# Performance work log

Measured on AMD Instinct MI355X. Metric: run time of the kernel, lower is better.

The kernel has to match this reference:

```python
import jax, jax.numpy as jnp
import numpy as np
import math

IN_CH = 256
OUT_CH = 256
N_JOINTS = 25
BATCH = 16384


def setup_inputs() -> dict:
    key = jax.random.key(0)
    kx, kw = jax.random.split(key)
    x = jax.random.normal(kx, (N_JOINTS, BATCH, IN_CH), dtype=jnp.float32)
    stdv = 1.0 / math.sqrt(OUT_CH)
    weight = jax.random.uniform(kw, (IN_CH, OUT_CH), dtype=jnp.float32,
                                minval=-stdv, maxval=stdv)
    return {"x": x, "weight": weight}


def reference(x, weight):
    # x: (N, B, D) -> attention over joints N per batch element
    xb = jnp.transpose(x, (1, 0, 2))            # (B, N, D)
    s3 = jnp.einsum('bnd,bmd->bnm', xb, xb)     # (B, N, N) self-similarity
    s = jax.nn.softmax(s3, axis=-1)
    out = jnp.einsum('bnm,bmd->bnd', s, xb)     # (B, N, D)
    out = out @ weight                           # (B, N, out_channels)
    return out
```

## Files before the change

### kernel.cpp

```cpp
#include <hip/hip_runtime.h>

#define GRID   512
#define BLOCK  512
#define BATCH  16384
#define NJ     25
#define DEPTH  256
#define ITERS  (BATCH / GRID)

typedef short s16x8 __attribute__((ext_vector_type(8)));
typedef short s16x4 __attribute__((ext_vector_type(4)));
typedef float f32x4 __attribute__((ext_vector_type(4)));

__device__ __forceinline__ short f2bf(float f) {
  union { float f; unsigned u; } c; c.f = f;
  unsigned r = (c.u + 0x7FFFu + ((c.u >> 16) & 1u)) >> 16;
  return (short)r;
}

#define MFMA(a, b, c) __builtin_amdgcn_mfma_f32_16x16x32_bf16((a), (b), (c), 0, 0, 0)

__global__ __launch_bounds__(BLOCK, 4)
void geo_gcn_fused(const float* __restrict__ x,
                   const float* __restrict__ w,
                   float* __restrict__ out)
{
  __shared__ short As[2][32][264];
  __shared__ short Ps[32][40];
  __shared__ float S3[32][33];
  __shared__ short Yt[8][32][40];

  const int tid  = threadIdx.x;
  const int wv   = tid >> 6;
  const int lane = tid & 63;
  const int quad = lane >> 4;
  const int l16  = lane & 15;

  s16x8 wf[8][2];
  {
    const int ncol = wv * 32 + l16;
#pragma unroll
    for (int ks = 0; ks < 8; ++ks)
#pragma unroll
      for (int td = 0; td < 2; ++td) {
        const float* wp = w + (size_t)(ks * 32 + quad * 8) * DEPTH + ncol + td * 16;
#pragma unroll
        for (int j = 0; j < 8; ++j)
          wf[ks][td][j] = f2bf(wp[(size_t)j * DEPTH]);
      }
  }

  const int srow = tid >> 4;
  const int sc   = tid & 15;
  const int tm_s = (wv >> 1) & 1;
  const int tn_s = wv & 1;

  const float* xrow = x + (size_t)srow * BATCH * DEPTH + sc * 16;

  {
    float4 c0 = make_float4(0.f, 0.f, 0.f, 0.f), c1 = c0, c2 = c0, c3 = c0;
    if (srow < NJ) {
      const float* xp = xrow + (size_t)blockIdx.x * DEPTH;
      c0 = *(const float4*)(xp + 0);  c1 = *(const float4*)(xp + 4);
      c2 = *(const float4*)(xp + 8);  c3 = *(const float4*)(xp + 12);
    }
    s16x8 h0, h1;
    h0[0]=f2bf(c0.x); h0[1]=f2bf(c0.y); h0[2]=f2bf(c0.z); h0[3]=f2bf(c0.w);
    h0[4]=f2bf(c1.x); h0[5]=f2bf(c1.y); h0[6]=f2bf(c1.z); h0[7]=f2bf(c1.w);
    h1[0]=f2bf(c2.x); h1[1]=f2bf(c2.y); h1[2]=f2bf(c2.z); h1[3]=f2bf(c2.w);
    h1[4]=f2bf(c3.x); h1[5]=f2bf(c3.y); h1[6]=f2bf(c3.z); h1[7]=f2bf(c3.w);
    *(s16x8*)&As[0][srow][sc * 16]     = h0;
    *(s16x8*)&As[0][srow][sc * 16 + 8] = h1;
  }
  __syncthreads();

  for (int ib = 0; ib < ITERS; ++ib) {
    const int b   = blockIdx.x + GRID * ib;
    const int buf = ib & 1;

    float4 n0 = make_float4(0.f, 0.f, 0.f, 0.f), n1 = n0, n2 = n0, n3 = n0;
    if ((ib + 1 < ITERS) && (srow < NJ)) {
      const float* xp = xrow + (size_t)(b + GRID) * DEPTH;
      n0 = *(const float4*)(xp + 0);  n1 = *(const float4*)(xp + 4);
      n2 = *(const float4*)(xp + 8);  n3 = *(const float4*)(xp + 12);
    }

    f32x4 sacc = (f32x4){0.f, 0.f, 0.f, 0.f};
    f32x4 yacc[2][2];
#pragma unroll
    for (int i = 0; i < 2; ++i)
#pragma unroll
      for (int j = 0; j < 2; ++j) yacc[i][j] = (f32x4){0.f, 0.f, 0.f, 0.f};

#pragma unroll
    for (int ks = 0; ks < 8; ++ks) {
      s16x8 a0 = *(const s16x8*)&As[buf][l16][ks * 32 + quad * 8];
      s16x8 a1 = *(const s16x8*)&As[buf][16 + l16][ks * 32 + quad * 8];
      if (wv < 4) sacc = MFMA(tm_s ? a1 : a0, tn_s ? a1 : a0, sacc);
      yacc[0][0] = MFMA(a0, wf[ks][0], yacc[0][0]);
      yacc[0][1] = MFMA(a0, wf[ks][1], yacc[0][1]);
      yacc[1][0] = MFMA(a1, wf[ks][0], yacc[1][0]);
      yacc[1][1] = MFMA(a1, wf[ks][1], yacc[1][1]);
    }

    if (wv < 4) {
#pragma unroll
      for (int r = 0; r < 4; ++r)
        S3[tm_s * 16 + quad * 4 + r][tn_s * 16 + l16] = sacc[r];
    }
    __syncthreads();

    if (tid < 256) {
      const int row = tid >> 3, c8 = tid & 7;
      float v[4]; float mx = -3.0e38f;
#pragma unroll
      for (int i = 0; i < 4; ++i) {
        const int j = c8 + 8 * i;
        v[i] = (j < NJ) ? S3[row][j] : -3.0e38f;
        mx = fmaxf(mx, v[i]);
      }
      mx = fmaxf(mx, __shfl_xor(mx, 1));
      mx = fmaxf(mx, __shfl_xor(mx, 2));
      mx = fmaxf(mx, __shfl_xor(mx, 4));
      float e[4]; float sum = 0.f;
#pragma unroll
      for (int i = 0; i < 4; ++i) {
        const int j = c8 + 8 * i;
        e[i] = (j < NJ) ? __expf(v[i] - mx) : 0.f;
        sum += e[i];
      }
      sum += __shfl_xor(sum, 1);
      sum += __shfl_xor(sum, 2);
      sum += __shfl_xor(sum, 4);
      const float rinv = 1.0f / sum;
#pragma unroll
      for (int i = 0; i < 4; ++i)
        Ps[row][c8 + 8 * i] = f2bf(e[i] * rinv);
    }
    __syncthreads();

#pragma unroll
    for (int tm = 0; tm < 2; ++tm)
#pragma unroll
      for (int td = 0; td < 2; ++td) {
        s16x4 hy;
#pragma unroll
        for (int r = 0; r < 4; ++r) hy[r] = f2bf(yacc[tm][td][r]);
        *(s16x4*)&Yt[wv][td * 16 + l16][tm * 16 + quad * 4] = hy;
      }

    s16x8 pf0 = *(const s16x8*)&Ps[l16][quad * 8];
    s16x8 pf1 = *(const s16x8*)&Ps[16 + l16][quad * 8];
    const f32x4 z4 = (f32x4){0.f, 0.f, 0.f, 0.f};
    float* ob = out + (size_t)b * NJ * DEPTH + wv * 32 + l16;
#pragma unroll
    for (int td = 0; td < 2; ++td) {
      s16x8 yb = *(const s16x8*)&Yt[wv][td * 16 + l16][quad * 8];
      f32x4 o0 = MFMA(pf0, yb, z4);
      f32x4 o1 = MFMA(pf1, yb, z4);
#pragma unroll
      for (int r = 0; r < 4; ++r) {
        ob[(size_t)(quad * 4 + r) * DEPTH + td * 16] = o0[r];
        const int nr = 16 + quad * 4 + r;
        if (nr < NJ) ob[(size_t)nr * DEPTH + td * 16] = o1[r];
      }
    }

    if (ib + 1 < ITERS) {
      s16x8 h0, h1;
      h0[0]=f2bf(n0.x); h0[1]=f2bf(n0.y); h0[2]=f2bf(n0.z); h0[3]=f2bf(n0.w);
      h0[4]=f2bf(n1.x); h0[5]=f2bf(n1.y); h0[6]=f2bf(n1.z); h0[7]=f2bf(n1.w);
      h1[0]=f2bf(n2.x); h1[1]=f2bf(n2.y); h1[2]=f2bf(n2.z); h1[3]=f2bf(n2.w);
      h1[4]=f2bf(n3.x); h1[5]=f2bf(n3.y); h1[6]=f2bf(n3.z); h1[7]=f2bf(n3.w);
      *(s16x8*)&As[1 - buf][srow][sc * 16]     = h0;
      *(s16x8*)&As[1 - buf][srow][sc * 16 + 8] = h1;
    }
    __syncthreads();
  }
}

extern "C" void kernel_launch(void* const* d_in, const int* in_sizes, int n_in,
                              void* d_out, int out_size, void* d_ws, size_t ws_size,
                              hipStream_t stream) {
  (void)in_sizes; (void)n_in; (void)out_size; (void)d_ws; (void)ws_size;
  const float* x = (const float*)d_in[0];
  const float* w = (const float*)d_in[1];
  float* out = (float*)d_out;
  geo_gcn_fused<<<dim3(GRID), dim3(BLOCK), 0, stream>>>(x, w, out);
}
```

Measured before the change: 793.5 us.

## Single-buffer swizzled LDS tiles and drop the end-of-iteration barrier

```diff
diff --git a/kernel.cpp b/kernel.cpp
--- a/kernel.cpp
+++ b/kernel.cpp
@@ -24,10 +24,10 @@
                    const float* __restrict__ w,
                    float* __restrict__ out)
 {
-  __shared__ short As[2][32][264];
+  __shared__ short As[32][256];
   __shared__ short Ps[32][40];
   __shared__ float S3[32][33];
-  __shared__ short Yt[8][32][40];
+  __shared__ short Yt[8][32][32];
 
   const int tid  = threadIdx.x;
   const int wv   = tid >> 6;
@@ -49,17 +49,19 @@
       }
   }
 
+  const int tm_s = (wv >> 1) & 1;
+  const int tn_s = wv & 1;
   const int srow = tid >> 4;
   const int sc   = tid & 15;
-  const int tm_s = (wv >> 1) & 1;
-  const int tn_s = wv & 1;
+  const int sw0  = ((2 * sc)     ^ (srow & 7)) * 8;
+  const int sw1  = ((2 * sc + 1) ^ (srow & 7)) * 8;
 
-  const float* xrow = x + (size_t)srow * BATCH * DEPTH + sc * 16;
+  const float* xb = x + (size_t)srow * BATCH * DEPTH + sc * 16;
 
   {
-    float4 c0 = make_float4(0.f, 0.f, 0.f, 0.f), c1 = c0, c2 = c0, c3 = c0;
+    float4 c0 = make_float4(0.f,0.f,0.f,0.f), c1 = c0, c2 = c0, c3 = c0;
     if (srow < NJ) {
-      const float* xp = xrow + (size_t)blockIdx.x * DEPTH;
+      const float* xp = xb + (size_t)blockIdx.x * DEPTH;
       c0 = *(const float4*)(xp + 0);  c1 = *(const float4*)(xp + 4);
       c2 = *(const float4*)(xp + 8);  c3 = *(const float4*)(xp + 12);
     }
@@ -68,20 +70,19 @@
     h0[4]=f2bf(c1.x); h0[5]=f2bf(c1.y); h0[6]=f2bf(c1.z); h0[7]=f2bf(c1.w);
     h1[0]=f2bf(c2.x); h1[1]=f2bf(c2.y); h1[2]=f2bf(c2.z); h1[3]=f2bf(c2.w);
     h1[4]=f2bf(c3.x); h1[5]=f2bf(c3.y); h1[6]=f2bf(c3.z); h1[7]=f2bf(c3.w);
-    *(s16x8*)&As[0][srow][sc * 16]     = h0;
-    *(s16x8*)&As[0][srow][sc * 16 + 8] = h1;
+    *(s16x8*)&As[srow][sw0] = h0;
+    *(s16x8*)&As[srow][sw1] = h1;
   }
   __syncthreads();
 
   for (int ib = 0; ib < ITERS; ++ib) {
-    const int b   = blockIdx.x + GRID * ib;
-    const int buf = ib & 1;
+    const int b = blockIdx.x + GRID * ib;
 
-    float4 n0 = make_float4(0.f, 0.f, 0.f, 0.f), n1 = n0, n2 = n0, n3 = n0;
+    float4 nf0 = make_float4(0.f,0.f,0.f,0.f), nf1 = nf0, nf2 = nf0, nf3 = nf0;
     if ((ib + 1 < ITERS) && (srow < NJ)) {
-      const float* xp = xrow + (size_t)(b + GRID) * DEPTH;
-      n0 = *(const float4*)(xp + 0);  n1 = *(const float4*)(xp + 4);
-      n2 = *(const float4*)(xp + 8);  n3 = *(const float4*)(xp + 12);
+      const float* xp = xb + (size_t)(b + GRID) * DEPTH;
+      nf0 = *(const float4*)(xp + 0);  nf1 = *(const float4*)(xp + 4);
+      nf2 = *(const float4*)(xp + 8);  nf3 = *(const float4*)(xp + 12);
     }
 
     f32x4 sacc = (f32x4){0.f, 0.f, 0.f, 0.f};
@@ -93,8 +94,9 @@
 
 #pragma unroll
     for (int ks = 0; ks < 8; ++ks) {
-      s16x8 a0 = *(const s16x8*)&As[buf][l16][ks * 32 + quad * 8];
-      s16x8 a1 = *(const s16x8*)&As[buf][16 + l16][ks * 32 + quad * 8];
+      const int co = (((ks * 4 + quad) ^ (l16 & 7)) << 3);
+      s16x8 a0 = *(const s16x8*)&As[l16][co];
+      s16x8 a1 = *(const s16x8*)&As[16 + l16][co];
       if (wv < 4) sacc = MFMA(tm_s ? a1 : a0, tn_s ? a1 : a0, sacc);
       yacc[0][0] = MFMA(a0, wf[ks][0], yacc[0][0]);
       yacc[0][1] = MFMA(a0, wf[ks][1], yacc[0][1]);
@@ -108,6 +110,16 @@
         S3[tm_s * 16 + quad * 4 + r][tn_s * 16 + l16] = sacc[r];
     }
     __syncthreads();
+
+    if (ib + 1 < ITERS) {
+      s16x8 h0, h1;
+      h0[0]=f2bf(nf0.x); h0[1]=f2bf(nf0.y); h0[2]=f2bf(nf0.z); h0[3]=f2bf(nf0.w);
+      h0[4]=f2bf(nf1.x); h0[5]=f2bf(nf1.y); h0[6]=f2bf(nf1.z); h0[7]=f2bf(nf1.w);
+      h1[0]=f2bf(nf2.x); h1[1]=f2bf(nf2.y); h1[2]=f2bf(nf2.z); h1[3]=f2bf(nf2.w);
+      h1[4]=f2bf(nf3.x); h1[5]=f2bf(nf3.y); h1[6]=f2bf(nf3.z); h1[7]=f2bf(nf3.w);
+      *(s16x8*)&As[srow][sw0] = h0;
+      *(s16x8*)&As[srow][sw1] = h1;
+    }
 
     if (tid < 256) {
       const int row = tid >> 3, c8 = tid & 7;
@@ -145,7 +157,8 @@
         s16x4 hy;
 #pragma unroll
         for (int r = 0; r < 4; ++r) hy[r] = f2bf(yacc[tm][td][r]);
-        *(s16x4*)&Yt[wv][td * 16 + l16][tm * 16 + quad * 4] = hy;
+        const int pc = ((tm * 2 + (quad >> 1)) ^ (l16 & 3)) * 8 + (quad & 1) * 4;
+        *(s16x4*)&Yt[wv][td * 16 + l16][pc] = hy;
       }
 
     s16x8 pf0 = *(const s16x8*)&Ps[l16][quad * 8];
@@ -154,7 +167,8 @@
     float* ob = out + (size_t)b * NJ * DEPTH + wv * 32 + l16;
 #pragma unroll
     for (int td = 0; td < 2; ++td) {
-      s16x8 yb = *(const s16x8*)&Yt[wv][td * 16 + l16][quad * 8];
+      const int rc = (quad ^ (l16 & 3)) * 8;
+      s16x8 yb = *(const s16x8*)&Yt[wv][td * 16 + l16][rc];
       f32x4 o0 = MFMA(pf0, yb, z4);
       f32x4 o1 = MFMA(pf1, yb, z4);
 #pragma unroll
@@ -164,17 +178,6 @@
         if (nr < NJ) ob[(size_t)nr * DEPTH + td * 16] = o1[r];
       }
     }
-
-    if (ib + 1 < ITERS) {
-      s16x8 h0, h1;
-      h0[0]=f2bf(n0.x); h0[1]=f2bf(n0.y); h0[2]=f2bf(n0.z); h0[3]=f2bf(n0.w);
-      h0[4]=f2bf(n1.x); h0[5]=f2bf(n1.y); h0[6]=f2bf(n1.z); h0[7]=f2bf(n1.w);
-      h1[0]=f2bf(n2.x); h1[1]=f2bf(n2.y); h1[2]=f2bf(n2.z); h1[3]=f2bf(n2.w);
-      h1[4]=f2bf(n3.x); h1[5]=f2bf(n3.y); h1[6]=f2bf(n3.z); h1[7]=f2bf(n3.w);
-      *(s16x8*)&As[1 - buf][srow][sc * 16]     = h0;
-      *(s16x8*)&As[1 - buf][srow][sc * 16 + 8] = h1;
-    }
-    __syncthreads();
   }
 }
 
```

Measured after the change: 848.4 us. 1.07x slower.
